# Kernel optimization log

Measured on AMD Instinct MI355X. Metric: run time of the kernel, lower is better.

The kernel has to match this reference:

```python
import jax, jax.numpy as jnp
import numpy as np

D_MODEL = 1024
NUM_LAYERS = 4
D_STATE = 64
D_CONV = 4
EXPAND = 2
HEADDIM = 64  # headdim = d_state per the module
D_INNER = EXPAND * D_MODEL              # 2048
NHEADS = D_INNER // HEADDIM             # 32
CONV_DIM = D_INNER + 2 * D_STATE        # 2176 (x, B, C)
D_IN_PROJ = 2 * D_INNER + 2 * D_STATE + NHEADS  # 4384 (z, xBC, dt)
EPS = 1e-5


def setup_inputs() -> dict:
    key = jax.random.key(0)
    ks = jax.random.split(key, 8)
    B, L = 4, 2048
    x = jax.random.normal(ks[0], (B, L, D_MODEL), dtype=jnp.float32)
    # stacked per-layer parameters
    in_w = jax.random.normal(ks[1], (NUM_LAYERS, D_MODEL, D_IN_PROJ), dtype=jnp.float32) * 0.02
    conv_w = (jax.random.uniform(ks[2], (NUM_LAYERS, D_CONV, CONV_DIM), dtype=jnp.float32) - 0.5) * (2.0 / np.sqrt(D_CONV))
    conv_b = jnp.zeros((NUM_LAYERS, CONV_DIM), dtype=jnp.float32)
    # dt init as in mamba-ssm: dt ~ exp(U * (log(0.1)-log(0.001)) + log(0.001)), dt_bias = inv_softplus(dt)
    u = jax.random.uniform(ks[3], (NUM_LAYERS, NHEADS), dtype=jnp.float32)
    dt = jnp.exp(u * (np.log(0.1) - np.log(0.001)) + np.log(0.001))
    dt_bias = dt + jnp.log(-jnp.expm1(-dt))
    A_log = jnp.log(jax.random.uniform(ks[4], (NUM_LAYERS, NHEADS), dtype=jnp.float32, minval=1.0, maxval=16.0))
    Dp = jnp.ones((NUM_LAYERS, NHEADS), dtype=jnp.float32)
    norm_w = jnp.ones((NUM_LAYERS, D_INNER), dtype=jnp.float32)
    out_w = jax.random.normal(ks[5], (NUM_LAYERS, D_INNER, D_MODEL), dtype=jnp.float32) * 0.02
    ln_w = jnp.ones((NUM_LAYERS, D_MODEL), dtype=jnp.float32)
    ln_b = jnp.zeros((NUM_LAYERS, D_MODEL), dtype=jnp.float32)
    return {"x": x, "ln_w": ln_w, "ln_b": ln_b, "in_w": in_w, "conv_w": conv_w,
            "conv_b": conv_b, "dt_bias": dt_bias, "A_log": A_log, "Dp": Dp,
            "norm_w": norm_w, "out_w": out_w}


def _layernorm(x, w, b):
    mu = jnp.mean(x, axis=-1, keepdims=True)
    xc = x - mu
    var = jnp.mean(xc * xc, axis=-1, keepdims=True)
    return xc * jax.lax.rsqrt(var + EPS) * w + b


def _mamba2(x, in_w, conv_w, conv_b, dt_bias, A_log, Dp, norm_w, out_w):
    Bb, L, _ = x.shape
    zxbcdt = jnp.einsum('bld,de->ble', x, in_w)            # (B,L,D_IN_PROJ)
    z = zxbcdt[..., :D_INNER]                               # (B,L,D_INNER)
    xBC = zxbcdt[..., D_INNER:D_INNER + CONV_DIM]           # (B,L,CONV_DIM)
    dt = jax.nn.softplus(zxbcdt[..., -NHEADS:] + dt_bias)   # (B,L,H)
    # causal depthwise conv1d (kernel D_CONV) + SiLU
    xp = jnp.pad(xBC, ((0, 0), (D_CONV - 1, 0), (0, 0)))
    conv = conv_b + sum(xp[:, k:k + L, :] * conv_w[k] for k in range(D_CONV))
    xBC = jax.nn.silu(conv)
    xs = xBC[..., :D_INNER].reshape(Bb, L, NHEADS, HEADDIM)  # (B,L,H,P)
    Bm = xBC[..., D_INNER:D_INNER + D_STATE]                 # (B,L,N), ngroups=1
    Cm = xBC[..., D_INNER + D_STATE:]                        # (B,L,N)
    A = -jnp.exp(A_log)                                      # (H,)
    dA = jnp.exp(dt * A)                                     # (B,L,H) decay per step
    dBx = dt[..., None] * xs                                 # (B,L,H,P)
    # selective state-space scan: h_t = dA_t*h_{t-1} + dBx_t (x) B_t ; y_t = h_t . C_t
    def step(h, t_in):
        dA_t, dBx_t, B_t, C_t = t_in
        h = h * dA_t[:, :, None, None] + dBx_t[..., None] * B_t[:, None, None, :]
        y = jnp.einsum('bhpn,bn->bhp', h, C_t)
        return h, y
    h0 = jnp.zeros((Bb, NHEADS, HEADDIM, D_STATE), x.dtype)
    xsT = (jnp.moveaxis(dA, 1, 0), jnp.moveaxis(dBx, 1, 0),
           jnp.moveaxis(Bm, 1, 0), jnp.moveaxis(Cm, 1, 0))
    _, yT = jax.lax.scan(step, h0, xsT)
    y = jnp.moveaxis(yT, 0, 1)                               # (B,L,H,P)
    y = y + Dp[None, None, :, None] * xs                     # skip via per-head D
    y = y.reshape(Bb, L, D_INNER)
    # gated RMSNorm (norm_before_gate=False): rmsnorm(y * silu(z)) * w
    y = y * jax.nn.silu(z)
    y = y * jax.lax.rsqrt(jnp.mean(y * y, axis=-1, keepdims=True) + EPS) * norm_w
    return jnp.einsum('ble,ed->bld', y, out_w)


def reference(x, ln_w, ln_b, in_w, conv_w, conv_b, dt_bias, A_log, Dp, norm_w, out_w):
    for i in range(NUM_LAYERS):
        xn = _layernorm(x, ln_w[i], ln_b[i])
        x = x + _mamba2(xn, in_w[i], conv_w[i], conv_b[i], dt_bias[i],
                        A_log[i], Dp[i], norm_w[i], out_w[i])
    return x
```

## Files before the change

### kernel.cpp

```cpp
#include <hip/hip_runtime.h>
#include <math.h>

#define LSEQ   2048
#define NROWS  8192
#define DMODEL 1024
#define DINNER 2048
#define NH     32
#define CONVD  2176
#define NPROJ  4256
#define NPROJ_PAD 4352
#define EPSV   1e-5f
#define SEGS   16
#define TSEG   128

typedef __bf16 bf16x8_t __attribute__((ext_vector_type(8)));
typedef float f32x4_t __attribute__((ext_vector_type(4)));
typedef unsigned short u16x8_t __attribute__((ext_vector_type(8)));

__device__ __forceinline__ unsigned short f2bf(float f) {
  unsigned int u = __float_as_uint(f);
  u += 0x7fffu + ((u >> 16) & 1u);
  return (unsigned short)(u >> 16);
}
__device__ __forceinline__ float bf2f(unsigned short u) {
  return __uint_as_float((unsigned int)u << 16);
}
__device__ __forceinline__ float siluf(float x) { return x / (1.f + expf(-x)); }

__device__ __forceinline__ void gload16(const unsigned short* g, unsigned short* l) {
  __builtin_amdgcn_global_load_lds(
      (const __attribute__((address_space(1))) void*)g,
      (__attribute__((address_space(3))) void*)l, 16, 0, 0);
}

__global__ __launch_bounds__(256) void ln_kernel(const float* __restrict__ X,
    const float* __restrict__ w, const float* __restrict__ b,
    unsigned short* __restrict__ out)
{
  const int r = blockIdx.x, tid = threadIdx.x;
  __shared__ float red[4];
  const float4 v = ((const float4*)(X + (size_t)r * DMODEL))[tid];
  float s = v.x + v.y + v.z + v.w;
#pragma unroll
  for (int o = 32; o > 0; o >>= 1) s += __shfl_down(s, o);
  if ((tid & 63) == 0) red[tid >> 6] = s;
  __syncthreads();
  const float mu = (red[0] + red[1] + red[2] + red[3]) * (1.f / DMODEL);
  __syncthreads();
  const float dx = v.x - mu, dy = v.y - mu, dz = v.z - mu, dw = v.w - mu;
  float ss = dx * dx + dy * dy + dz * dz + dw * dw;
#pragma unroll
  for (int o = 32; o > 0; o >>= 1) ss += __shfl_down(ss, o);
  if ((tid & 63) == 0) red[tid >> 6] = ss;
  __syncthreads();
  const float var = (red[0] + red[1] + red[2] + red[3]) * (1.f / DMODEL);
  const float rs = rsqrtf(var + EPSV);
  const float4 wv = ((const float4*)w)[tid];
  const float4 bv = ((const float4*)b)[tid];
  const size_t d = (size_t)r * DMODEL + tid * 4;
  out[d + 0] = f2bf(dx * rs * wv.x + bv.x);
  out[d + 1] = f2bf(dy * rs * wv.y + bv.y);
  out[d + 2] = f2bf(dz * rs * wv.z + bv.z);
  out[d + 3] = f2bf(dw * rs * wv.w + bv.w);
}

__global__ void transpose_bf16(const float* __restrict__ W,
    unsigned short* __restrict__ WT, int K, int N)
{
  __shared__ float t[32][33];
  const int n0 = blockIdx.x * 32, k0 = blockIdx.y * 32;
  const int tx = threadIdx.x, ty = threadIdx.y;
  if (n0 + tx < N) t[ty][tx] = W[(size_t)(k0 + ty) * N + n0 + tx];
  __syncthreads();
  if (n0 + ty < N) WT[(size_t)(n0 + ty) * K + k0 + tx] = f2bf(t[tx][ty]);
}

#define STAGE(BUF, KT) do {                                        \
    const int kt_ = (KT) * 32;                                     \
    gload16(Ag + kt_,                  sA##BUF + tid * 8);         \
    gload16(Ag + (size_t)64 * K + kt_, sA##BUF + 2048 + tid * 8);  \
    gload16(Bg + kt_,                  sB##BUF + tid * 8);         \
    gload16(Bg + (size_t)64 * K + kt_, sB##BUF + 2048 + tid * 8);  \
  } while (0)

#define COMPUTE(BUF) do {                                                           \
    bf16x8_t af[4], bfr[4];                                                         \
    _Pragma("unroll")                                                               \
    for (int mi = 0; mi < 4; ++mi)                                                  \
      af[mi] = *(const bf16x8_t*)(sA##BUF + (wr * 64 + mi * 16 + la) * 32 + lb * 8);\
    _Pragma("unroll")                                                               \
    for (int ni = 0; ni < 4; ++ni)                                                  \
      bfr[ni] = *(const bf16x8_t*)(sB##BUF + (wc * 64 + ni * 16 + la) * 32 + lb * 8);\
    _Pragma("unroll")                                                               \
    for (int mi = 0; mi < 4; ++mi)                                                  \
      _Pragma("unroll")                                                             \
      for (int ni = 0; ni < 4; ++ni)                                                \
        acc[mi][ni] = __builtin_amdgcn_mfma_f32_16x16x32_bf16(af[mi], bfr[ni],      \
                                                              acc[mi][ni], 0, 0, 0);\
  } while (0)

#define WAITBAR(N) do {                                          \
    __builtin_amdgcn_sched_barrier(0);                           \
    asm volatile("s_waitcnt vmcnt(" #N ")" ::: "memory");        \
    __builtin_amdgcn_s_barrier();                                \
    __builtin_amdgcn_sched_barrier(0);                           \
  } while (0)

#define BAR do {                                 \
    __builtin_amdgcn_sched_barrier(0);           \
    __builtin_amdgcn_s_barrier();                \
    __builtin_amdgcn_sched_barrier(0);           \
  } while (0)

__global__ __launch_bounds__(256) void gemm_bf16(
    const unsigned short* __restrict__ A,
    const unsigned short* __restrict__ BT,
    float* __restrict__ Cf,
    unsigned short* __restrict__ Cb,
    int N, int K, int ldc)
{
  __shared__ __attribute__((aligned(16))) unsigned short sA0[128 * 32];
  __shared__ __attribute__((aligned(16))) unsigned short sA1[128 * 32];
  __shared__ __attribute__((aligned(16))) unsigned short sB0[128 * 32];
  __shared__ __attribute__((aligned(16))) unsigned short sB1[128 * 32];
  const int tid = threadIdx.x;
  const int w = tid >> 6, l = tid & 63;
  const int wr = w >> 1, wc = w & 1;
  const int la = l & 15, lb = l >> 4;
  const int m0 = blockIdx.x * 128, n0 = blockIdx.y * 128;
  f32x4_t acc[4][4];
#pragma unroll
  for (int i = 0; i < 4; ++i)
#pragma unroll
    for (int j = 0; j < 4; ++j) acc[i][j] = (f32x4_t){0.f, 0.f, 0.f, 0.f};

  const int r0 = tid >> 2, q0 = tid & 3;
  const unsigned short* Ag = A + (size_t)(m0 + r0) * K + q0 * 8;
  const unsigned short* Bg = BT + (size_t)(n0 + r0) * K + q0 * 8;
  const int nkt = K / 32;

  STAGE(0, 0);
  STAGE(1, 1);

  for (int t = 0; t < nkt - 2; t += 2) {
    WAITBAR(4);
    COMPUTE(0);
    BAR;
    STAGE(0, t + 2);
    WAITBAR(4);
    COMPUTE(1);
    BAR;
    STAGE(1, t + 3);
  }
  WAITBAR(4);
  COMPUTE(0);
  WAITBAR(0);
  COMPUTE(1);

#pragma unroll
  for (int mi = 0; mi < 4; ++mi) {
#pragma unroll
    for (int ni = 0; ni < 4; ++ni) {
      const int col = n0 + wc * 64 + ni * 16 + la;
      if (col < N) {
#pragma unroll
        for (int r = 0; r < 4; ++r) {
          const int row = m0 + wr * 64 + mi * 16 + lb * 4 + r;
          const size_t idx = (size_t)row * ldc + col;
          const float v = acc[mi][ni][r];
          if (Cb) Cb[idx] = f2bf(v);
          else    Cf[idx] += v;
        }
      }
    }
  }
}

__global__ __launch_bounds__(256) void conv_kernel(const unsigned short* __restrict__ zx,
    const float* __restrict__ cw, const float* __restrict__ cb,
    unsigned short* __restrict__ out)
{
  const int c8 = (blockIdx.x * 256 + threadIdx.x) * 8;
  if (c8 >= CONVD) return;
  const int r = blockIdx.y;
  const int l = r & (LSEQ - 1);
  float acc[8];
  {
    const float4 b0 = *(const float4*)(cb + c8);
    const float4 b1 = *(const float4*)(cb + c8 + 4);
    acc[0] = b0.x; acc[1] = b0.y; acc[2] = b0.z; acc[3] = b0.w;
    acc[4] = b1.x; acc[5] = b1.y; acc[6] = b1.z; acc[7] = b1.w;
  }
#pragma unroll
  for (int k = 0; k < 4; ++k) {
    if (l + k - 3 >= 0) {
      const u16x8_t v = *(const u16x8_t*)(zx + (size_t)(r + k - 3) * NPROJ + DINNER + c8);
      const float4 w0 = *(const float4*)(cw + k * CONVD + c8);
      const float4 w1 = *(const float4*)(cw + k * CONVD + c8 + 4);
      acc[0] = fmaf(bf2f(v[0]), w0.x, acc[0]);
      acc[1] = fmaf(bf2f(v[1]), w0.y, acc[1]);
      acc[2] = fmaf(bf2f(v[2]), w0.z, acc[2]);
      acc[3] = fmaf(bf2f(v[3]), w0.w, acc[3]);
      acc[4] = fmaf(bf2f(v[4]), w1.x, acc[4]);
      acc[5] = fmaf(bf2f(v[5]), w1.y, acc[5]);
      acc[6] = fmaf(bf2f(v[6]), w1.z, acc[6]);
      acc[7] = fmaf(bf2f(v[7]), w1.w, acc[7]);
    }
  }
  u16x8_t o;
#pragma unroll
  for (int j = 0; j < 8; ++j) o[j] = f2bf(siluf(acc[j]));
  *(u16x8_t*)(out + (size_t)r * CONVD + c8) = o;
}

#define CBB(t, cbyte)  ((char*)CB  + (t) * 256 + ((cbyte) ^ (((t) & 7) << 4)))
#define XTB(p, cbyte)  ((char*)Xt  + (p) * 256 + ((cbyte) ^ (((p) & 7) << 4)))
#define BTWB(n, cbyte) ((char*)Btw + (n) * 256 + ((cbyte) ^ (((n) & 7) << 4)))
__global__ __launch_bounds__(256) void ssd_chunk_kernel(
    const unsigned short* __restrict__ xbc,
    const unsigned short* __restrict__ zraw,
    const float* __restrict__ dt_bias,
    const float* __restrict__ A_log,
    const float* __restrict__ Dp,
    unsigned short* __restrict__ y, int ldy,
    unsigned short* __restrict__ H,
    float* __restrict__ cumdec)
{
  __shared__ unsigned short CB[TSEG * 128];
  __shared__ unsigned short Xt[64 * TSEG];
  __shared__ unsigned short Btw[64 * TSEG];
  __shared__ float cumS[TSEG], dtS[TSEG], wS[TSEG];
  const int id = blockIdx.x;
  const int bh = id >> 4, ch = id & 15;
  const int b = bh >> 5, h = bh & 31;
  const int tid = threadIdx.x;
  const int w = tid >> 6, l = tid & 63;
  const int la = l & 15, lb = l >> 4;
  const size_t row0 = (size_t)b * LSEQ + (size_t)ch * TSEG;
  const unsigned short* xr = xbc + row0 * CONVD;
  const float dp = Dp[h];

  {
    const int t = tid >> 1, q = tid & 1;
    const unsigned short* src = xr + (size_t)t * CONVD;
#pragma unroll
    for (int j = 0; j < 4; ++j) {
      const int c0 = q * 32 + j * 8;
      *(u16x8_t*)CBB(t, c0 * 2)       = *(const u16x8_t*)(src + 2112 + c0);
      *(u16x8_t*)CBB(t, 128 + c0 * 2) = *(const u16x8_t*)(src + 2048 + c0);
      const u16x8_t xv = *(const u16x8_t*)(src + h * 64 + c0);
#pragma unroll
      for (int e = 0; e < 8; ++e)
        *(unsigned short*)XTB(c0 + e, t * 2) = xv[e];
    }
  }
  if (w == 0) {
    const float bias = dt_bias[h];
    const float aexp = __expf(A_log[h]);
    const float x0 = bf2f(zraw[(row0 + l) * NPROJ + (DINNER + CONVD) + h]) + bias;
    const float x1 = bf2f(zraw[(row0 + 64 + l) * NPROJ + (DINNER + CONVD) + h]) + bias;
    const float d0 = (x0 > 20.f) ? x0 : log1pf(__expf(x0));
    const float d1 = (x1 > 20.f) ? x1 : log1pf(__expf(x1));
    float a0 = -d0 * aexp;
    float a1 = -d1 * aexp;
#pragma unroll
    for (int o = 1; o < 64; o <<= 1) { const float u = __shfl_up(a0, o); if (l >= o) a0 += u; }
    const float tot0 = __shfl(a0, 63);
#pragma unroll
    for (int o = 1; o < 64; o <<= 1) { const float u = __shfl_up(a1, o); if (l >= o) a1 += u; }
    a1 += tot0;
    const float cT = __shfl(a1, 63);
    cumS[l] = a0;       cumS[64 + l] = a1;
    dtS[l] = d0;        dtS[64 + l] = d1;
    wS[l] = __expf(cT - a0) * d0;
    wS[64 + l] = __expf(cT - a1) * d1;
    float* cdg = cumdec + (size_t)bh * LSEQ + (size_t)ch * TSEG;
    cdg[l] = __expf(a0);
    cdg[64 + l] = __expf(a1);
  }
  __syncthreads();

  f32x4_t g[2][8];
#pragma unroll
  for (int mi = 0; mi < 2; ++mi)
#pragma unroll
    for (int ni = 0; ni < 8; ++ni) g[mi][ni] = (f32x4_t){0.f, 0.f, 0.f, 0.f};
#pragma unroll
  for (int ks = 0; ks < 2; ++ks) {
    bf16x8_t af[2], bfr[8];
#pragma unroll
    for (int mi = 0; mi < 2; ++mi)
      af[mi] = *(const bf16x8_t*)CBB(w * 32 + mi * 16 + la, ks * 64 + lb * 16);
#pragma unroll
    for (int ni = 0; ni < 8; ++ni)
      bfr[ni] = *(const bf16x8_t*)CBB(ni * 16 + la, 128 + ks * 64 + lb * 16);
#pragma unroll
    for (int mi = 0; mi < 2; ++mi)
#pragma unroll
      for (int ni = 0; ni < 8; ++ni)
        g[mi][ni] = __builtin_amdgcn_mfma_f32_16x16x32_bf16(af[mi], bfr[ni], g[mi][ni], 0, 0, 0);
  }
  __syncthreads();

#pragma unroll
  for (int mi = 0; mi < 2; ++mi) {
#pragma unroll
    for (int ni = 0; ni < 8; ++ni) {
      const int s = ni * 16 + la;
#pragma unroll
      for (int r = 0; r < 4; ++r) {
        const int t = w * 32 + mi * 16 + lb * 4 + r;
        float mv = 0.f;
        if (s <= t) mv = g[mi][ni][r] * __expf(cumS[t] - cumS[s]) * dtS[s];
        if (s == t) mv += dp;
        *(unsigned short*)CBB(t, s * 2) = f2bf(mv);
      }
    }
  }
  {
    const int s = tid >> 1, q = tid & 1;
    const unsigned short* src = xr + (size_t)s * CONVD + 2048;
    const float ww = wS[s];
#pragma unroll
    for (int j = 0; j < 4; ++j) {
      const int c0 = q * 32 + j * 8;
      const u16x8_t bv = *(const u16x8_t*)(src + c0);
#pragma unroll
      for (int e = 0; e < 8; ++e)
        *(unsigned short*)BTWB(c0 + e, s * 2) = f2bf(bf2f(bv[e]) * ww);
    }
  }
  __syncthreads();

  f32x4_t y1[2][4];
#pragma unroll
  for (int mi = 0; mi < 2; ++mi)
#pragma unroll
    for (int ni = 0; ni < 4; ++ni) y1[mi][ni] = (f32x4_t){0.f, 0.f, 0.f, 0.f};
#pragma unroll
  for (int ks = 0; ks < 4; ++ks) {
    bf16x8_t af[2], xf[4];
#pragma unroll
    for (int mi = 0; mi < 2; ++mi)
      af[mi] = *(const bf16x8_t*)CBB(w * 32 + mi * 16 + la, ks * 64 + lb * 16);
#pragma unroll
    for (int ni = 0; ni < 4; ++ni)
      xf[ni] = *(const bf16x8_t*)XTB(ni * 16 + la, ks * 64 + lb * 16);
#pragma unroll
    for (int mi = 0; mi < 2; ++mi)
#pragma unroll
      for (int ni = 0; ni < 4; ++ni)
        y1[mi][ni] = __builtin_amdgcn_mfma_f32_16x16x32_bf16(af[mi], xf[ni], y1[mi][ni], 0, 0, 0);
  }
  f32x4_t hacc[4];
#pragma unroll
  for (int ni = 0; ni < 4; ++ni) hacc[ni] = (f32x4_t){0.f, 0.f, 0.f, 0.f};
#pragma unroll
  for (int ks = 0; ks < 4; ++ks) {
    const bf16x8_t af = *(const bf16x8_t*)XTB(w * 16 + la, ks * 64 + lb * 16);
    bf16x8_t bw[4];
#pragma unroll
    for (int ni = 0; ni < 4; ++ni)
      bw[ni] = *(const bf16x8_t*)BTWB(ni * 16 + la, ks * 64 + lb * 16);
#pragma unroll
    for (int ni = 0; ni < 4; ++ni)
      hacc[ni] = __builtin_amdgcn_mfma_f32_16x16x32_bf16(af, bw[ni], hacc[ni], 0, 0, 0);
  }

  unsigned short* yg = y + row0 * ldy + h * 64;
#pragma unroll
  for (int mi = 0; mi < 2; ++mi)
#pragma unroll
    for (int ni = 0; ni < 4; ++ni)
#pragma unroll
      for (int r = 0; r < 4; ++r) {
        const int t = w * 32 + mi * 16 + lb * 4 + r;
        yg[(size_t)t * ldy + ni * 16 + la] = f2bf(y1[mi][ni][r]);
      }
  unsigned short* Hg = H + ((size_t)ch * 128 + bh) * 4096;
#pragma unroll
  for (int ni = 0; ni < 4; ++ni)
#pragma unroll
    for (int r = 0; r < 4; ++r) {
      const int p = w * 16 + lb * 4 + r;
      Hg[p * 64 + ni * 16 + la] = f2bf(hacc[ni][r]);
    }
}

__global__ __launch_bounds__(256) void scan2_kernel(
    unsigned short* __restrict__ H, const float* __restrict__ cumdec)
{
  const int bh = blockIdx.x;
  const int e = threadIdx.x * 16;
  float hs[16];
#pragma unroll
  for (int k = 0; k < 16; ++k) hs[k] = 0.f;
  unsigned short* Hb = H + (size_t)bh * 4096 + e;
  const float* cd = cumdec + (size_t)bh * LSEQ;
  for (int s = 0; s < SEGS; ++s) {
    unsigned short* p = Hb + (size_t)s * 128 * 4096;
    const float rseg = cd[s * TSEG + TSEG - 1];
    u16x8_t v0 = *(u16x8_t*)p, v1 = *(u16x8_t*)(p + 8);
    u16x8_t w0, w1;
#pragma unroll
    for (int k = 0; k < 8; ++k) {
      const float tmp = bf2f(v0[k]);
      w0[k] = f2bf(hs[k]);
      hs[k] = fmaf(rseg, hs[k], tmp);
    }
#pragma unroll
    for (int k = 0; k < 8; ++k) {
      const float tmp = bf2f(v1[k]);
      w1[k] = f2bf(hs[k + 8]);
      hs[k + 8] = fmaf(rseg, hs[k + 8], tmp);
    }
    *(u16x8_t*)p = w0;
    *(u16x8_t*)(p + 8) = w1;
  }
}

#define CSB(t, cbyte) ((char*)Cs + (t) * 128 + ((cbyte) ^ (((t) & 7) << 4)))
#define HSB(p, cbyte) ((char*)Hs + (p) * 128 + ((cbyte) ^ (((p) & 7) << 4)))
__global__ __launch_bounds__(256) void scan3_mfma(
    const unsigned short* __restrict__ xbc,
    const float* __restrict__ cumdec,
    const unsigned short* __restrict__ H,
    unsigned short* __restrict__ y, int ldy)
{
  __shared__ unsigned short Cs[TSEG * 64];
  __shared__ unsigned short Hs[64 * 64];
  __shared__ float cdS[TSEG];
  const int id = blockIdx.x;
  const int bh = id / 15, ch = id % 15 + 1;
  const int b = bh >> 5, h = bh & 31;
  const int tid = threadIdx.x, w = tid >> 6, l = tid & 63;
  const int la = l & 15, lb = l >> 4;
  const size_t row0 = (size_t)b * LSEQ + (size_t)ch * TSEG;
  const unsigned short* xr = xbc + row0 * CONVD;
  {
    const int t = tid >> 1, q = tid & 1;
#pragma unroll
    for (int j = 0; j < 4; ++j) {
      const int c0 = q * 32 + j * 8;
      *(u16x8_t*)CSB(t, c0 * 2) = *(const u16x8_t*)(xr + (size_t)t * CONVD + 2112 + c0);
    }
  }
  {
    const int p = tid >> 2, q = tid & 3;
    const unsigned short* hsrc = H + ((size_t)ch * 128 + bh) * 4096 + p * 64;
#pragma unroll
    for (int j = 0; j < 2; ++j) {
      const int c0 = q * 16 + j * 8;
      *(u16x8_t*)HSB(p, c0 * 2) = *(const u16x8_t*)(hsrc + c0);
    }
  }
  if (tid < TSEG) cdS[tid] = cumdec[(size_t)bh * LSEQ + (size_t)ch * TSEG + tid];
  __syncthreads();
  f32x4_t acc[2][4];
#pragma unroll
  for (int mi = 0; mi < 2; ++mi)
#pragma unroll
    for (int ni = 0; ni < 4; ++ni) acc[mi][ni] = (f32x4_t){0.f, 0.f, 0.f, 0.f};
#pragma unroll
  for (int ks = 0; ks < 2; ++ks) {
    bf16x8_t af[2], bfr[4];
#pragma unroll
    for (int mi = 0; mi < 2; ++mi)
      af[mi] = *(const bf16x8_t*)CSB(w * 32 + mi * 16 + la, ks * 64 + lb * 16);
#pragma unroll
    for (int ni = 0; ni < 4; ++ni)
      bfr[ni] = *(const bf16x8_t*)HSB(ni * 16 + la, ks * 64 + lb * 16);
#pragma unroll
    for (int mi = 0; mi < 2; ++mi)
#pragma unroll
      for (int ni = 0; ni < 4; ++ni)
        acc[mi][ni] = __builtin_amdgcn_mfma_f32_16x16x32_bf16(af[mi], bfr[ni], acc[mi][ni], 0, 0, 0);
  }
  unsigned short* yg = y + row0 * ldy + h * 64;
#pragma unroll
  for (int mi = 0; mi < 2; ++mi)
#pragma unroll
    for (int ni = 0; ni < 4; ++ni)
#pragma unroll
      for (int r = 0; r < 4; ++r) {
        const int t = w * 32 + mi * 16 + lb * 4 + r;
        unsigned short* yp = yg + (size_t)t * ldy + ni * 16 + la;
        *yp = f2bf(bf2f(*yp) + acc[mi][ni][r] * cdS[t]);
      }
}

__global__ __launch_bounds__(256) void gate_kernel(const unsigned short* __restrict__ zx,
    const float* __restrict__ nw, unsigned short* __restrict__ out)
{
  const int r = blockIdx.x, tid = threadIdx.x;
  __shared__ float red[4];
  const size_t rb = (size_t)r * NPROJ;
  const u16x8_t zv = *(const u16x8_t*)(zx + rb + tid * 8);
  const u16x8_t yv = *(const u16x8_t*)(zx + rb + 2048 + tid * 8);
  float v[8];
#pragma unroll
  for (int i = 0; i < 8; ++i) v[i] = bf2f(yv[i]) * siluf(bf2f(zv[i]));
  float ss = 0.f;
#pragma unroll
  for (int i = 0; i < 8; ++i) ss += v[i] * v[i];
#pragma unroll
  for (int o = 32; o > 0; o >>= 1) ss += __shfl_down(ss, o);
  if ((tid & 63) == 0) red[tid >> 6] = ss;
  __syncthreads();
  const float var = (red[0] + red[1] + red[2] + red[3]) * (1.f / DINNER);
  const float rs = rsqrtf(var + EPSV);
  const float4 w0 = ((const float4*)nw)[tid * 2];
  const float4 w1 = ((const float4*)nw)[tid * 2 + 1];
  u16x8_t o;
  o[0] = f2bf(v[0] * rs * w0.x); o[1] = f2bf(v[1] * rs * w0.y);
  o[2] = f2bf(v[2] * rs * w0.z); o[3] = f2bf(v[3] * rs * w0.w);
  o[4] = f2bf(v[4] * rs * w1.x); o[5] = f2bf(v[5] * rs * w1.y);
  o[6] = f2bf(v[6] * rs * w1.z); o[7] = f2bf(v[7] * rs * w1.w);
  *(u16x8_t*)(out + (size_t)r * DINNER + tid * 8) = o;
}

extern "C" void kernel_launch(void* const* d_in, const int* in_sizes, int n_in,
                              void* d_out, int out_size, void* d_ws, size_t ws_size,
                              hipStream_t stream) {
  (void)in_sizes; (void)n_in; (void)out_size; (void)ws_size;
  const float* x_in    = (const float*)d_in[0];
  const float* ln_w    = (const float*)d_in[1];
  const float* ln_b    = (const float*)d_in[2];
  const float* in_w    = (const float*)d_in[3];
  const float* conv_w  = (const float*)d_in[4];
  const float* conv_b  = (const float*)d_in[5];
  const float* dt_bias = (const float*)d_in[6];
  const float* A_log   = (const float*)d_in[7];
  const float* Dp      = (const float*)d_in[8];
  const float* norm_w  = (const float*)d_in[9];
  const float* out_w   = (const float*)d_in[10];
  float* xout = (float*)d_out;

  char* ws = (char*)d_ws;
  unsigned short* zxb  = (unsigned short*)ws;
  char* r1 = ws + (size_t)NROWS * NPROJ * 2;
  unsigned short* xn   = (unsigned short*)r1;
  unsigned short* xbcb = (unsigned short*)r1;
  unsigned short* ybf  = (unsigned short*)r1;
  char* wth = r1 + (size_t)NROWS * CONVD * 2;
  unsigned short* inwT = (unsigned short*)wth;
  unsigned short* owT  = (unsigned short*)wth;
  unsigned short* Hbuf = (unsigned short*)wth;
  float* cumdec = (float*)(wth + (size_t)SEGS * 128 * 4096 * 2);

  hipMemcpyAsync(xout, x_in, (size_t)NROWS * DMODEL * 4, hipMemcpyDeviceToDevice, stream);

  for (int i = 0; i < 4; ++i) {
    ln_kernel<<<NROWS, 256, 0, stream>>>(xout, ln_w + i * DMODEL, ln_b + i * DMODEL, xn);
    transpose_bf16<<<dim3(133, 32), dim3(32, 32), 0, stream>>>(
        in_w + (size_t)i * DMODEL * NPROJ, inwT, DMODEL, NPROJ);
    gemm_bf16<<<dim3(64, 34), 256, 0, stream>>>(xn, inwT, nullptr, zxb, NPROJ, DMODEL, NPROJ);
    conv_kernel<<<dim3(2, NROWS), 256, 0, stream>>>(
        zxb, conv_w + (size_t)i * 4 * CONVD, conv_b + i * CONVD, xbcb);
    ssd_chunk_kernel<<<128 * SEGS, 256, 0, stream>>>(xbcb, zxb,
        dt_bias + i * NH, A_log + i * NH, Dp + i * NH,
        zxb + 2048, NPROJ, Hbuf, cumdec);
    scan2_kernel<<<128, 256, 0, stream>>>(Hbuf, cumdec);
    scan3_mfma<<<128 * 15, 256, 0, stream>>>(xbcb, cumdec, Hbuf, zxb + 2048, NPROJ);
    gate_kernel<<<NROWS, 256, 0, stream>>>(zxb, norm_w + i * DINNER, ybf);
    transpose_bf16<<<dim3(32, 64), dim3(32, 32), 0, stream>>>(
        out_w + (size_t)i * DINNER * DMODEL, owT, DINNER, DMODEL);
    gemm_bf16<<<dim3(64, 8), 256, 0, stream>>>(ybf, owT, xout, nullptr, DMODEL, DINNER, DMODEL);
  }
}
```

Before: 1.352 ms.

## Fuse depthwise conv+SiLU into SSD kernels and swizzle GEMM block order

Removes the standalone conv kernel and its intermediate xBC buffer. The causal depthwise conv and SiLU are now recomputed inside ssd_chunk_kernel and scan3_mfma straight from the projection output. A small halo kernel first copies the three x rows before each chunk boundary, because y is written in place over the x columns of zxb. The GEMMs switch to a 1D grid with a block-index swizzle meant to improve L2 locality. The trade is redundant conv arithmetic and extra global loads of weights and B/C rows inside the SSD kernels, in exchange for one fewer launch and one fewer full read/write pass.

New measurement: 1.648 ms. 1.22x slower.

```diff
diff --git a/kernel.cpp b/kernel.cpp
--- a/kernel.cpp
+++ b/kernel.cpp
@@ -117,7 +117,7 @@
     const unsigned short* __restrict__ BT,
     float* __restrict__ Cf,
     unsigned short* __restrict__ Cb,
-    int N, int K, int ldc)
+    int N, int K, int ldc, int gx)
 {
   __shared__ __attribute__((aligned(16))) unsigned short sA0[128 * 32];
   __shared__ __attribute__((aligned(16))) unsigned short sA1[128 * 32];
@@ -127,7 +127,9 @@
   const int w = tid >> 6, l = tid & 63;
   const int wr = w >> 1, wc = w & 1;
   const int la = l & 15, lb = l >> 4;
-  const int m0 = blockIdx.x * 128, n0 = blockIdx.y * 128;
+  const int nwg = gridDim.x;
+  const int swz = (blockIdx.x & 7) * (nwg >> 3) + (blockIdx.x >> 3);
+  const int m0 = (swz % gx) * 128, n0 = (swz / gx) * 128;
   f32x4_t acc[4][4];
 #pragma unroll
   for (int i = 0; i < 4; ++i)
@@ -176,49 +178,24 @@
   }
 }
 
-__global__ __launch_bounds__(256) void conv_kernel(const unsigned short* __restrict__ zx,
-    const float* __restrict__ cw, const float* __restrict__ cb,
-    unsigned short* __restrict__ out)
-{
-  const int c8 = (blockIdx.x * 256 + threadIdx.x) * 8;
-  if (c8 >= CONVD) return;
-  const int r = blockIdx.y;
-  const int l = r & (LSEQ - 1);
-  float acc[8];
-  {
-    const float4 b0 = *(const float4*)(cb + c8);
-    const float4 b1 = *(const float4*)(cb + c8 + 4);
-    acc[0] = b0.x; acc[1] = b0.y; acc[2] = b0.z; acc[3] = b0.w;
-    acc[4] = b1.x; acc[5] = b1.y; acc[6] = b1.z; acc[7] = b1.w;
-  }
-#pragma unroll
-  for (int k = 0; k < 4; ++k) {
-    if (l + k - 3 >= 0) {
-      const u16x8_t v = *(const u16x8_t*)(zx + (size_t)(r + k - 3) * NPROJ + DINNER + c8);
-      const float4 w0 = *(const float4*)(cw + k * CONVD + c8);
-      const float4 w1 = *(const float4*)(cw + k * CONVD + c8 + 4);
-      acc[0] = fmaf(bf2f(v[0]), w0.x, acc[0]);
-      acc[1] = fmaf(bf2f(v[1]), w0.y, acc[1]);
-      acc[2] = fmaf(bf2f(v[2]), w0.z, acc[2]);
-      acc[3] = fmaf(bf2f(v[3]), w0.w, acc[3]);
-      acc[4] = fmaf(bf2f(v[4]), w1.x, acc[4]);
-      acc[5] = fmaf(bf2f(v[5]), w1.y, acc[5]);
-      acc[6] = fmaf(bf2f(v[6]), w1.z, acc[6]);
-      acc[7] = fmaf(bf2f(v[7]), w1.w, acc[7]);
-    }
-  }
-  u16x8_t o;
-#pragma unroll
-  for (int j = 0; j < 8; ++j) o[j] = f2bf(siluf(acc[j]));
-  *(u16x8_t*)(out + (size_t)r * CONVD + c8) = o;
+__global__ __launch_bounds__(256) void halo_kernel(
+    const unsigned short* __restrict__ zxb, unsigned short* __restrict__ halo)
+{
+  const int id = blockIdx.x;
+  const int bb = id / 45, rem = id % 45;
+  const int ch = rem / 3 + 1, rr = rem % 3;
+  const size_t row = (size_t)bb * LSEQ + (size_t)ch * TSEG - 3 + rr;
+  const u16x8_t v = *(const u16x8_t*)(zxb + row * NPROJ + 2048 + threadIdx.x * 8);
+  *(u16x8_t*)(halo + (size_t)id * 2048 + threadIdx.x * 8) = v;
 }
 
 #define CBB(t, cbyte)  ((char*)CB  + (t) * 256 + ((cbyte) ^ (((t) & 7) << 4)))
 #define XTB(p, cbyte)  ((char*)Xt  + (p) * 256 + ((cbyte) ^ (((p) & 7) << 4)))
 #define BTWB(n, cbyte) ((char*)Btw + (n) * 256 + ((cbyte) ^ (((n) & 7) << 4)))
 __global__ __launch_bounds__(256) void ssd_chunk_kernel(
-    const unsigned short* __restrict__ xbc,
-    const unsigned short* __restrict__ zraw,
+    const unsigned short* __restrict__ zxb,
+    const unsigned short* __restrict__ halo,
+    const float* __restrict__ cw, const float* __restrict__ cb,
     const float* __restrict__ dt_bias,
     const float* __restrict__ A_log,
     const float* __restrict__ Dp,
@@ -237,28 +214,87 @@
   const int w = tid >> 6, l = tid & 63;
   const int la = l & 15, lb = l >> 4;
   const size_t row0 = (size_t)b * LSEQ + (size_t)ch * TSEG;
-  const unsigned short* xr = xbc + row0 * CONVD;
   const float dp = Dp[h];
 
   {
     const int t = tid >> 1, q = tid & 1;
-    const unsigned short* src = xr + (size_t)t * CONVD;
+    const unsigned short* pX[4];
+    const unsigned short* pBC[4];
+#pragma unroll
+    for (int k = 0; k < 4; ++k) {
+      const int tk = t + k;
+      if (ch == 0 && tk < 3) { pX[k] = nullptr; pBC[k] = nullptr; }
+      else {
+        const size_t g = row0 + tk - 3;
+        pBC[k] = zxb + g * NPROJ + 4096;
+        pX[k]  = (tk < 3)
+            ? (halo + ((size_t)((b * 15 + ch - 1) * 3 + tk)) * 2048 + h * 64)
+            : (zxb + g * NPROJ + 2048 + h * 64);
+      }
+    }
 #pragma unroll
     for (int j = 0; j < 4; ++j) {
       const int c0 = q * 32 + j * 8;
-      *(u16x8_t*)CBB(t, c0 * 2)       = *(const u16x8_t*)(src + 2112 + c0);
-      *(u16x8_t*)CBB(t, 128 + c0 * 2) = *(const u16x8_t*)(src + 2048 + c0);
-      const u16x8_t xv = *(const u16x8_t*)(src + h * 64 + c0);
+      float xa[8], ba[8], ca[8];
+      {
+        const float4 x0 = *(const float4*)(cb + h * 64 + c0);
+        const float4 x1 = *(const float4*)(cb + h * 64 + c0 + 4);
+        const float4 b0 = *(const float4*)(cb + 2048 + c0);
+        const float4 b1 = *(const float4*)(cb + 2048 + c0 + 4);
+        const float4 c0v = *(const float4*)(cb + 2112 + c0);
+        const float4 c1v = *(const float4*)(cb + 2112 + c0 + 4);
+        xa[0]=x0.x; xa[1]=x0.y; xa[2]=x0.z; xa[3]=x0.w;
+        xa[4]=x1.x; xa[5]=x1.y; xa[6]=x1.z; xa[7]=x1.w;
+        ba[0]=b0.x; ba[1]=b0.y; ba[2]=b0.z; ba[3]=b0.w;
+        ba[4]=b1.x; ba[5]=b1.y; ba[6]=b1.z; ba[7]=b1.w;
+        ca[0]=c0v.x; ca[1]=c0v.y; ca[2]=c0v.z; ca[3]=c0v.w;
+        ca[4]=c1v.x; ca[5]=c1v.y; ca[6]=c1v.z; ca[7]=c1v.w;
+      }
+#pragma unroll
+      for (int k = 0; k < 4; ++k) {
+        if (pBC[k]) {
+          const u16x8_t xv = *(const u16x8_t*)(pX[k] + c0);
+          const u16x8_t bv = *(const u16x8_t*)(pBC[k] + c0);
+          const u16x8_t cv = *(const u16x8_t*)(pBC[k] + 64 + c0);
+          const float* wk = cw + k * CONVD;
+          const float4 xw0 = *(const float4*)(wk + h * 64 + c0);
+          const float4 xw1 = *(const float4*)(wk + h * 64 + c0 + 4);
+          const float4 bw0 = *(const float4*)(wk + 2048 + c0);
+          const float4 bw1 = *(const float4*)(wk + 2048 + c0 + 4);
+          const float4 cw0 = *(const float4*)(wk + 2112 + c0);
+          const float4 cw1 = *(const float4*)(wk + 2112 + c0 + 4);
+          xa[0]=fmaf(bf2f(xv[0]),xw0.x,xa[0]); xa[1]=fmaf(bf2f(xv[1]),xw0.y,xa[1]);
+          xa[2]=fmaf(bf2f(xv[2]),xw0.z,xa[2]); xa[3]=fmaf(bf2f(xv[3]),xw0.w,xa[3]);
+          xa[4]=fmaf(bf2f(xv[4]),xw1.x,xa[4]); xa[5]=fmaf(bf2f(xv[5]),xw1.y,xa[5]);
+          xa[6]=fmaf(bf2f(xv[6]),xw1.z,xa[6]); xa[7]=fmaf(bf2f(xv[7]),xw1.w,xa[7]);
+          ba[0]=fmaf(bf2f(bv[0]),bw0.x,ba[0]); ba[1]=fmaf(bf2f(bv[1]),bw0.y,ba[1]);
+          ba[2]=fmaf(bf2f(bv[2]),bw0.z,ba[2]); ba[3]=fmaf(bf2f(bv[3]),bw0.w,ba[3]);
+          ba[4]=fmaf(bf2f(bv[4]),bw1.x,ba[4]); ba[5]=fmaf(bf2f(bv[5]),bw1.y,ba[5]);
+          ba[6]=fmaf(bf2f(bv[6]),bw1.z,ba[6]); ba[7]=fmaf(bf2f(bv[7]),bw1.w,ba[7]);
+          ca[0]=fmaf(bf2f(cv[0]),cw0.x,ca[0]); ca[1]=fmaf(bf2f(cv[1]),cw0.y,ca[1]);
+          ca[2]=fmaf(bf2f(cv[2]),cw0.z,ca[2]); ca[3]=fmaf(bf2f(cv[3]),cw0.w,ca[3]);
+          ca[4]=fmaf(bf2f(cv[4]),cw1.x,ca[4]); ca[5]=fmaf(bf2f(cv[5]),cw1.y,ca[5]);
+          ca[6]=fmaf(bf2f(cv[6]),cw1.z,ca[6]); ca[7]=fmaf(bf2f(cv[7]),cw1.w,ca[7]);
+        }
+      }
+      u16x8_t co, bo;
+#pragma unroll
+      for (int e = 0; e < 8; ++e) {
+        co[e] = f2bf(siluf(ca[e]));
+        bo[e] = f2bf(siluf(ba[e]));
+      }
+      *(u16x8_t*)CBB(t, c0 * 2)       = co;
+      *(u16x8_t*)CBB(t, 128 + c0 * 2) = bo;
 #pragma unroll
       for (int e = 0; e < 8; ++e)
-        *(unsigned short*)XTB(c0 + e, t * 2) = xv[e];
+        *(unsigned short*)XTB(c0 + e, t * 2) = f2bf(siluf(xa[e]));
     }
   }
   if (w == 0) {
     const float bias = dt_bias[h];
     const float aexp = __expf(A_log[h]);
-    const float x0 = bf2f(zraw[(row0 + l) * NPROJ + (DINNER + CONVD) + h]) + bias;
-    const float x1 = bf2f(zraw[(row0 + 64 + l) * NPROJ + (DINNER + CONVD) + h]) + bias;
+    const float x0 = bf2f(zxb[(row0 + l) * NPROJ + (DINNER + CONVD) + h]) + bias;
+    const float x1 = bf2f(zxb[(row0 + 64 + l) * NPROJ + (DINNER + CONVD) + h]) + bias;
     const float d0 = (x0 > 20.f) ? x0 : log1pf(__expf(x0));
     const float d1 = (x1 > 20.f) ? x1 : log1pf(__expf(x1));
     float a0 = -d0 * aexp;
@@ -302,6 +338,20 @@
   }
   __syncthreads();
 
+  {
+    const int s = tid >> 1, q = tid & 1;
+    const float ww = wS[s];
+#pragma unroll
+    for (int j = 0; j < 4; ++j) {
+      const int c0 = q * 32 + j * 8;
+      const u16x8_t bv = *(const u16x8_t*)CBB(s, 128 + c0 * 2);
+#pragma unroll
+      for (int e = 0; e < 8; ++e)
+        *(unsigned short*)BTWB(c0 + e, s * 2) = f2bf(bf2f(bv[e]) * ww);
+    }
+  }
+  __syncthreads();
+
 #pragma unroll
   for (int mi = 0; mi < 2; ++mi) {
 #pragma unroll
@@ -315,19 +365,6 @@
         if (s == t) mv += dp;
         *(unsigned short*)CBB(t, s * 2) = f2bf(mv);
       }
-    }
-  }
-  {
-    const int s = tid >> 1, q = tid & 1;
-    const unsigned short* src = xr + (size_t)s * CONVD + 2048;
-    const float ww = wS[s];
-#pragma unroll
-    for (int j = 0; j < 4; ++j) {
-      const int c0 = q * 32 + j * 8;
-      const u16x8_t bv = *(const u16x8_t*)(src + c0);
-#pragma unroll
-      for (int e = 0; e < 8; ++e)
-        *(unsigned short*)BTWB(c0 + e, s * 2) = f2bf(bf2f(bv[e]) * ww);
     }
   }
   __syncthreads();
@@ -422,7 +459,8 @@
 #define CSB(t, cbyte) ((char*)Cs + (t) * 128 + ((cbyte) ^ (((t) & 7) << 4)))
 #define HSB(p, cbyte) ((char*)Hs + (p) * 128 + ((cbyte) ^ (((p) & 7) << 4)))
 __global__ __launch_bounds__(256) void scan3_mfma(
-    const unsigned short* __restrict__ xbc,
+    const unsigned short* __restrict__ zxb,
+    const float* __restrict__ cw, const float* __restrict__ cb,
     const float* __restrict__ cumdec,
     const unsigned short* __restrict__ H,
     unsigned short* __restrict__ y, int ldy)
@@ -436,13 +474,32 @@
   const int tid = threadIdx.x, w = tid >> 6, l = tid & 63;
   const int la = l & 15, lb = l >> 4;
   const size_t row0 = (size_t)b * LSEQ + (size_t)ch * TSEG;
-  const unsigned short* xr = xbc + row0 * CONVD;
   {
     const int t = tid >> 1, q = tid & 1;
 #pragma unroll
     for (int j = 0; j < 4; ++j) {
       const int c0 = q * 32 + j * 8;
-      *(u16x8_t*)CSB(t, c0 * 2) = *(const u16x8_t*)(xr + (size_t)t * CONVD + 2112 + c0);
+      float acc[8];
+      {
+        const float4 b0 = *(const float4*)(cb + 2112 + c0);
+        const float4 b1 = *(const float4*)(cb + 2112 + c0 + 4);
+        acc[0]=b0.x; acc[1]=b0.y; acc[2]=b0.z; acc[3]=b0.w;
+        acc[4]=b1.x; acc[5]=b1.y; acc[6]=b1.z; acc[7]=b1.w;
+      }
+#pragma unroll
+      for (int k = 0; k < 4; ++k) {
+        const u16x8_t v = *(const u16x8_t*)(zxb + (row0 + t + k - 3) * NPROJ + 4160 + c0);
+        const float4 w0 = *(const float4*)(cw + k * CONVD + 2112 + c0);
+        const float4 w1 = *(const float4*)(cw + k * CONVD + 2112 + c0 + 4);
+        acc[0]=fmaf(bf2f(v[0]),w0.x,acc[0]); acc[1]=fmaf(bf2f(v[1]),w0.y,acc[1]);
+        acc[2]=fmaf(bf2f(v[2]),w0.z,acc[2]); acc[3]=fmaf(bf2f(v[3]),w0.w,acc[3]);
+        acc[4]=fmaf(bf2f(v[4]),w1.x,acc[4]); acc[5]=fmaf(bf2f(v[5]),w1.y,acc[5]);
+        acc[6]=fmaf(bf2f(v[6]),w1.z,acc[6]); acc[7]=fmaf(bf2f(v[7]),w1.w,acc[7]);
+      }
+      u16x8_t o;
+#pragma unroll
+      for (int e = 0; e < 8; ++e) o[e] = f2bf(siluf(acc[e]));
+      *(u16x8_t*)CSB(t, c0 * 2) = o;
     }
   }
   {
@@ -540,31 +597,33 @@
   unsigned short* zxb  = (unsigned short*)ws;
   char* r1 = ws + (size_t)NROWS * NPROJ * 2;
   unsigned short* xn   = (unsigned short*)r1;
-  unsigned short* xbcb = (unsigned short*)r1;
   unsigned short* ybf  = (unsigned short*)r1;
   char* wth = r1 + (size_t)NROWS * CONVD * 2;
   unsigned short* inwT = (unsigned short*)wth;
   unsigned short* owT  = (unsigned short*)wth;
   unsigned short* Hbuf = (unsigned short*)wth;
   float* cumdec = (float*)(wth + (size_t)SEGS * 128 * 4096 * 2);
+  unsigned short* halo = (unsigned short*)((char*)cumdec + (size_t)128 * LSEQ * 4);
 
   hipMemcpyAsync(xout, x_in, (size_t)NROWS * DMODEL * 4, hipMemcpyDeviceToDevice, stream);
 
   for (int i = 0; i < 4; ++i) {
+    const float* cw_i = conv_w + (size_t)i * 4 * CONVD;
+    const float* cb_i = conv_b + (size_t)i * CONVD;
     ln_kernel<<<NROWS, 256, 0, stream>>>(xout, ln_w + i * DMODEL, ln_b + i * DMODEL, xn);
     transpose_bf16<<<dim3(133, 32), dim3(32, 32), 0, stream>>>(
         in_w + (size_t)i * DMODEL * NPROJ, inwT, DMODEL, NPROJ);
-    gemm_bf16<<<dim3(64, 34), 256, 0, stream>>>(xn, inwT, nullptr, zxb, NPROJ, DMODEL, NPROJ);
-    conv_kernel<<<dim3(2, NROWS), 256, 0, stream>>>(
-        zxb, conv_w + (size_t)i * 4 * CONVD, conv_b + i * CONVD, xbcb);
-    ssd_chunk_kernel<<<128 * SEGS, 256, 0, stream>>>(xbcb, zxb,
+    gemm_bf16<<<64 * 34, 256, 0, stream>>>(xn, inwT, nullptr, zxb, NPROJ, DMODEL, NPROJ, 64);
+    halo_kernel<<<180, 256, 0, stream>>>(zxb, halo);
+    ssd_chunk_kernel<<<128 * SEGS, 256, 0, stream>>>(zxb, halo, cw_i, cb_i,
         dt_bias + i * NH, A_log + i * NH, Dp + i * NH,
         zxb + 2048, NPROJ, Hbuf, cumdec);
     scan2_kernel<<<128, 256, 0, stream>>>(Hbuf, cumdec);
-    scan3_mfma<<<128 * 15, 256, 0, stream>>>(xbcb, cumdec, Hbuf, zxb + 2048, NPROJ);
+    scan3_mfma<<<128 * 15, 256, 0, stream>>>(zxb, cw_i, cb_i, cumdec, Hbuf,
+                                             zxb + 2048, NPROJ);
     gate_kernel<<<NROWS, 256, 0, stream>>>(zxb, norm_w + i * DINNER, ybf);
     transpose_bf16<<<dim3(32, 64), dim3(32, 32), 0, stream>>>(
         out_w + (size_t)i * DINNER * DMODEL, owT, DINNER, DMODEL);
-    gemm_bf16<<<dim3(64, 8), 256, 0, stream>>>(ybf, owT, xout, nullptr, DMODEL, DINNER, DMODEL);
-  }
-}
+    gemm_bf16<<<64 * 8, 256, 0, stream>>>(ybf, owT, xout, nullptr, DMODEL, DINNER, DMODEL, 64);
+  }
+}
```
